# Optimization experiments

Hardware: AMD Instinct MI355X
Metric: run time of the kernel (lower is better)

## Reference

```python
import jax, jax.numpy as jnp
import numpy as np

B, SQ, SK, H, NH = 2, 2048, 2048, 1024, 16
HD = H // NH  # 64


def setup_inputs() -> dict:
    key = jax.random.key(0)
    ks = jax.random.split(key, 12)
    s = 1.0 / np.sqrt(H)
    inp = {
        "query": jax.random.normal(ks[0], (B, SQ, H), jnp.float32),
        "key": jax.random.normal(ks[1], (B, SK, H), jnp.float32),
        "value": jax.random.normal(ks[2], (B, SK, H), jnp.float32),
        # lower-triangular causal mask [B, SQ, SK]; nonzero = attend
        "causal_mask": jnp.broadcast_to(
            jnp.tril(jnp.ones((SQ, SK), jnp.int32)), (B, SQ, SK)
        ),
        "Wq": jax.random.uniform(ks[3], (H, H), jnp.float32, -s, s),
        "bq": jnp.zeros((H,), jnp.float32),
        "Wk": jax.random.uniform(ks[4], (H, H), jnp.float32, -s, s),
        "bk": jnp.zeros((H,), jnp.float32),
        "Wv": jax.random.uniform(ks[5], (H, H), jnp.float32, -s, s),
        "bv": jnp.zeros((H,), jnp.float32),
        "Wo": jax.random.uniform(ks[6], (H, H), jnp.float32, -s, s),
        "bo": jnp.zeros((H,), jnp.float32),
        "ln_g": jnp.ones((H,), jnp.float32),
        "ln_b": jnp.zeros((H,), jnp.float32),
    }
    return inp


def _layer_norm(x, g, b, eps=1e-5):
    mu = jnp.mean(x, axis=-1, keepdims=True)
    var = jnp.var(x, axis=-1, keepdims=True)
    return (x - mu) * jax.lax.rsqrt(var + eps) * g + b


def reference(query, key, value, causal_mask, Wq, bq, Wk, bk, Wv, bv, Wo, bo, ln_g, ln_b):
    # projections (torch Linear: x @ W.T + b)
    q = (query @ Wq.T + bq).reshape(B, SQ, NH, HD)
    k = (key @ Wk.T + bk).reshape(B, SK, NH, HD)
    v = (value @ Wv.T + bv).reshape(B, SK, NH, HD)
    # scores [B, NH, SQ, SK]
    scores = jnp.einsum("bqhd,bkhd->bhqk", q, k) / np.sqrt(HD).astype(np.float32)
    scores = jnp.where(causal_mask[:, None, :, :] == 0, -jnp.inf, scores)
    attn = jax.nn.softmax(scores, axis=-1)
    # dropout is identity in eval mode
    out = jnp.einsum("bhqk,bkhd->bqhd", attn, v).reshape(B, SQ, H)
    out = out @ Wo.T + bo
    return _layer_norm(query + out, ln_g, ln_b)
```

## Files before the change

kernel.cpp:

```cpp
#include <hip/hip_runtime.h>
#include <hip/hip_bf16.h>

#define SQL 2048
#define SKL 2048
#define HH  1024
#define NHH 16
#define HDD 64
#define BB  2
#define MM  (BB*SQL)

typedef __attribute__((ext_vector_type(8))) short short8;
typedef __attribute__((ext_vector_type(4))) short short4v;
typedef __attribute__((ext_vector_type(4))) float f32x4;
typedef unsigned short u16;

__device__ inline u16 f2bf(float f) {
    unsigned int u = __float_as_uint(f);
    u += 0x7fffu + ((u >> 16) & 1u);
    return (u16)(u >> 16);
}

__device__ inline void gl_lds16(const void* g, void* l) {
    __builtin_amdgcn_global_load_lds(
        (const __attribute__((address_space(1))) unsigned int*)g,
        (__attribute__((address_space(3))) unsigned int*)l, 16, 0, 0);
}

__global__ __launch_bounds__(256) void cvt_all_kernel(
    const float* __restrict__ q, const float* __restrict__ k, const float* __restrict__ v,
    const float* __restrict__ wq, const float* __restrict__ wk,
    const float* __restrict__ wv, const float* __restrict__ wo,
    u16* __restrict__ xq, u16* __restrict__ xk, u16* __restrict__ xv,
    u16* __restrict__ wqb, u16* __restrict__ wkb, u16* __restrict__ wvb, u16* __restrict__ wob)
{
    int b = blockIdx.x;
    const float* src; u16* dst;
    if      (b < 4096)  { src = q;  dst = xq; }
    else if (b < 8192)  { src = k;  dst = xk;  b -= 4096; }
    else if (b < 12288) { src = v;  dst = xv;  b -= 8192; }
    else if (b < 13312) { src = wq; dst = wqb; b -= 12288; }
    else if (b < 14336) { src = wk; dst = wkb; b -= 13312; }
    else if (b < 15360) { src = wv; dst = wvb; b -= 14336; }
    else                { src = wo; dst = wob; b -= 15360; }
    int i = (b * 256 + threadIdx.x) * 4;
    float4 vv = *(const float4*)(src + i);
    ushort4 oo;
    oo.x = f2bf(vv.x); oo.y = f2bf(vv.y); oo.z = f2bf(vv.z); oo.w = f2bf(vv.w);
    *(ushort4*)(dst + i) = oo;
}

__global__ __launch_bounds__(256) void proj_kernel(
    const u16* __restrict__ xq, const u16* __restrict__ xk, const u16* __restrict__ xv,
    const u16* __restrict__ wqb, const u16* __restrict__ wkb, const u16* __restrict__ wvb,
    const float* __restrict__ bq, const float* __restrict__ bk, const float* __restrict__ bv,
    u16* __restrict__ oq, u16* __restrict__ ok, u16* __restrict__ ov)
{
    const int z = blockIdx.z;
    const u16* A      = (z == 0) ? xq  : (z == 1) ? xk  : xv;
    const u16* W      = (z == 0) ? wqb : (z == 1) ? wkb : wvb;
    const float* bias = (z == 0) ? bq  : (z == 1) ? bk  : bv;
    u16* outb         = (z == 0) ? oq  : (z == 1) ? ok  : ov;
    const float scale = (z == 0) ? 0.125f * 1.4426950408889634f : 1.0f;

    __shared__ u16 lds_a[128 * 64];
    __shared__ u16 lds_b[128 * 64];

    const int t = threadIdx.x;
    const int lane = t & 63;
    const int quad = lane >> 4;
    const int lo = lane & 15;
    const int wv = t >> 6;
    const int wm = (wv >> 1) * 64, wn = (wv & 1) * 64;
    const int m0 = blockIdx.x * 128;
    const int n0 = blockIdx.y * 128;

    f32x4 acc[4][4];
#pragma unroll
    for (int i = 0; i < 4; i++)
#pragma unroll
        for (int j = 0; j < 4; j++) acc[i][j] = (f32x4){0.f, 0.f, 0.f, 0.f};

    int rr[4], cc[4];
#pragma unroll
    for (int u = 0; u < 4; u++) {
        int sl = u * 256 + t;
        rr[u] = sl >> 3;
        cc[u] = ((sl & 7) ^ (rr[u] & 7)) * 8;
    }

    for (int k0 = 0; k0 < HH; k0 += 64) {
#pragma unroll
        for (int u = 0; u < 4; u++) {
            gl_lds16(A + (size_t)(m0 + rr[u]) * HH + k0 + cc[u], &lds_a[(u * 256 + t) * 8]);
            gl_lds16(W + (size_t)(n0 + rr[u]) * HH + k0 + cc[u], &lds_b[(u * 256 + t) * 8]);
        }
        __syncthreads();
#pragma unroll
        for (int kk = 0; kk < 2; kk++) {
            short8 af[4], bf[4];
#pragma unroll
            for (int i = 0; i < 4; i++) {
                const int ra = wm + i * 16 + lo;
                const int rb = wn + i * 16 + lo;
                af[i] = *(const short8*)&lds_a[ra * 64 + (((kk * 4 + quad) ^ (ra & 7)) * 8)];
                bf[i] = *(const short8*)&lds_b[rb * 64 + (((kk * 4 + quad) ^ (rb & 7)) * 8)];
            }
            if (z == 2) {
#pragma unroll
                for (int i = 0; i < 4; i++)
#pragma unroll
                    for (int j = 0; j < 4; j++)
                        acc[i][j] = __builtin_amdgcn_mfma_f32_16x16x32_bf16(bf[j], af[i], acc[i][j], 0, 0, 0);
            } else {
#pragma unroll
                for (int i = 0; i < 4; i++)
#pragma unroll
                    for (int j = 0; j < 4; j++)
                        acc[i][j] = __builtin_amdgcn_mfma_f32_16x16x32_bf16(af[i], bf[j], acc[i][j], 0, 0, 0);
            }
        }
        __syncthreads();
    }

#pragma unroll
    for (int i = 0; i < 4; i++) {
#pragma unroll
        for (int j = 0; j < 4; j++) {
#pragma unroll
            for (int r = 0; r < 4; r++) {
                if (z == 2) {
                    int dg  = n0 + wn + j * 16 + quad * 4 + r;
                    int tok = m0 + wm + i * 16 + lo;
                    float val = acc[i][j][r] + bias[dg];
                    int head = dg >> 6, d = dg & 63;
                    int bi = tok >> 11, s = tok & 2047;
                    outb[(((size_t)bi * NHH + head) * HDD + d) * SKL + s] = f2bf(val);
                } else {
                    int row = m0 + wm + i * 16 + quad * 4 + r;
                    int col = n0 + wn + j * 16 + lo;
                    float val = (acc[i][j][r] + bias[col]) * scale;
                    int bi = row >> 11, s = row & 2047;
                    int head = col >> 6, d = col & 63;
                    outb[(((size_t)bi * NHH + head) * SQL + s) * HDD + d] = f2bf(val);
                }
            }
        }
    }
}

__global__ __launch_bounds__(256) void outproj_kernel(
    const u16* __restrict__ A, const u16* __restrict__ W,
    const float* __restrict__ bias, const float* __restrict__ resid,
    float* __restrict__ outf)
{
    __shared__ u16 lds_a[128 * 64];
    __shared__ u16 lds_b[128 * 64];

    const int t = threadIdx.x;
    const int lane = t & 63;
    const int quad = lane >> 4;
    const int lo = lane & 15;
    const int wv = t >> 6;
    const int wm = (wv >> 1) * 64, wn = (wv & 1) * 64;
    const int m0 = blockIdx.x * 128;
    const int n0 = blockIdx.y * 128;

    f32x4 acc[4][4];
#pragma unroll
    for (int i = 0; i < 4; i++)
#pragma unroll
        for (int j = 0; j < 4; j++) acc[i][j] = (f32x4){0.f, 0.f, 0.f, 0.f};

    int rr[4], cc[4];
#pragma unroll
    for (int u = 0; u < 4; u++) {
        int sl = u * 256 + t;
        rr[u] = sl >> 3;
        cc[u] = ((sl & 7) ^ (rr[u] & 7)) * 8;
    }

    for (int k0 = 0; k0 < HH; k0 += 64) {
#pragma unroll
        for (int u = 0; u < 4; u++) {
            gl_lds16(A + (size_t)(m0 + rr[u]) * HH + k0 + cc[u], &lds_a[(u * 256 + t) * 8]);
            gl_lds16(W + (size_t)(n0 + rr[u]) * HH + k0 + cc[u], &lds_b[(u * 256 + t) * 8]);
        }
        __syncthreads();
#pragma unroll
        for (int kk = 0; kk < 2; kk++) {
            short8 af[4], bf[4];
#pragma unroll
            for (int i = 0; i < 4; i++) {
                const int ra = wm + i * 16 + lo;
                const int rb = wn + i * 16 + lo;
                af[i] = *(const short8*)&lds_a[ra * 64 + (((kk * 4 + quad) ^ (ra & 7)) * 8)];
                bf[i] = *(const short8*)&lds_b[rb * 64 + (((kk * 4 + quad) ^ (rb & 7)) * 8)];
            }
#pragma unroll
            for (int i = 0; i < 4; i++)
#pragma unroll
                for (int j = 0; j < 4; j++)
                    acc[i][j] = __builtin_amdgcn_mfma_f32_16x16x32_bf16(af[i], bf[j], acc[i][j], 0, 0, 0);
        }
        __syncthreads();
    }

#pragma unroll
    for (int i = 0; i < 4; i++)
#pragma unroll
        for (int j = 0; j < 4; j++)
#pragma unroll
            for (int r = 0; r < 4; r++) {
                int row = m0 + wm + i * 16 + quad * 4 + r;
                int col = n0 + wn + j * 16 + lo;
                float val = acc[i][j][r] + bias[col] + resid[(size_t)row * HH + col];
                outf[(size_t)row * HH + col] = val;
            }
}

#define PSTR 72

__global__ __launch_bounds__(256) void attn_kernel(
    const u16* __restrict__ qb, const u16* __restrict__ kb, const u16* __restrict__ vtb,
    u16* __restrict__ attn_out)
{
    __shared__ u16 k_lds[64 * 64];
    __shared__ u16 vt_lds[64 * 64];
    __shared__ u16 p_lds[4 * 16 * PSTR];

    const int t = threadIdx.x;
    const int lane = t & 63;
    const int quad = lane >> 4;
    const int lo = lane & 15;
    const int w = t >> 6;
    const int qt = (SQL / 64 - 1) - (blockIdx.x >> 5);
    const int bh = blockIdx.x & 31;
    const int q0 = qt * 64;

    const u16* qbase = qb + ((size_t)bh * SQL + q0 + w * 16 + lo) * HDD + quad * 8;
    short8 qf0 = *(const short8*)qbase;
    short8 qf1 = *(const short8*)(qbase + 32);

    float m_s = -__builtin_inff(), l_s = 0.f;
    f32x4 o[4];
#pragma unroll
    for (int j = 0; j < 4; j++) o[j] = (f32x4){0.f, 0.f, 0.f, 0.f};

    const int sl0 = t, sl1 = 256 + t;
    const int r0 = sl0 >> 3, c0 = ((sl0 & 7) ^ (r0 & 7)) * 8;
    const int r1 = sl1 >> 3, c1 = ((sl1 & 7) ^ (r1 & 7)) * 8;
    const u16* kbh = kb + (size_t)bh * SKL * HDD;
    const u16* vbh = vtb + (size_t)bh * HDD * SKL;
    u16* ppriv = &p_lds[w * 16 * PSTR];

    for (int kt = 0; kt <= qt; kt++) {
        const int k0 = kt * 64;
        gl_lds16(kbh + (size_t)(k0 + r0) * HDD + c0, &k_lds[sl0 * 8]);
        gl_lds16(kbh + (size_t)(k0 + r1) * HDD + c1, &k_lds[sl1 * 8]);
        gl_lds16(vbh + (size_t)r0 * SKL + k0 + c0, &vt_lds[sl0 * 8]);
        gl_lds16(vbh + (size_t)r1 * SKL + k0 + c1, &vt_lds[sl1 * 8]);
        __syncthreads();

        f32x4 s[4];
        __builtin_amdgcn_s_setprio(1);
#pragma unroll
        for (int nt = 0; nt < 4; nt++) {
            const int row = nt * 16 + lo;
            short8 kf0 = *(const short8*)&k_lds[row * 64 + ((quad ^ (row & 7)) * 8)];
            short8 kf1 = *(const short8*)&k_lds[row * 64 + (((4 + quad) ^ (row & 7)) * 8)];
            s[nt] = (f32x4){0.f, 0.f, 0.f, 0.f};
            s[nt] = __builtin_amdgcn_mfma_f32_16x16x32_bf16(kf0, qf0, s[nt], 0, 0, 0);
            s[nt] = __builtin_amdgcn_mfma_f32_16x16x32_bf16(kf1, qf1, s[nt], 0, 0, 0);
        }
        __builtin_amdgcn_s_setprio(0);
        if (kt == qt) {
            const int ql = w * 16 + lo;
#pragma unroll
            for (int nt = 0; nt < 4; nt++)
#pragma unroll
                for (int r = 0; r < 4; r++)
                    if (nt * 16 + quad * 4 + r > ql) s[nt][r] = -__builtin_inff();
        }

        float mx = s[0][0];
#pragma unroll
        for (int nt = 0; nt < 4; nt++)
#pragma unroll
            for (int r = 0; r < 4; r++) mx = fmaxf(mx, s[nt][r]);
        mx = fmaxf(mx, __shfl_xor(mx, 16));
        mx = fmaxf(mx, __shfl_xor(mx, 32));

        if (!__all(mx - m_s <= 8.0f)) {
            float mnew = fmaxf(m_s, mx);
            float al = __builtin_amdgcn_exp2f(m_s - mnew);
            m_s = mnew;
            l_s *= al;
            float alr[4];
#pragma unroll
            for (int r = 0; r < 4; r++) alr[r] = __shfl(al, quad * 4 + r, 16);
#pragma unroll
            for (int nt = 0; nt < 4; nt++)
#pragma unroll
                for (int r = 0; r < 4; r++) o[nt][r] *= alr[r];
        }

        float rs = 0.f;
#pragma unroll
        for (int nt = 0; nt < 4; nt++)
#pragma unroll
            for (int r = 0; r < 4; r++) {
                s[nt][r] = __builtin_amdgcn_exp2f(s[nt][r] - m_s);
                rs += s[nt][r];
            }
        rs += __shfl_xor(rs, 16);
        rs += __shfl_xor(rs, 32);
        l_s += rs;

#pragma unroll
        for (int nt = 0; nt < 4; nt++) {
            short4v pk;
#pragma unroll
            for (int r = 0; r < 4; r++) pk[r] = (short)f2bf(s[nt][r]);
            *(short4v*)&ppriv[lo * PSTR + nt * 16 + quad * 4] = pk;
        }
        short8 pf0 = *(const short8*)&ppriv[lo * PSTR + quad * 8];
        short8 pf1 = *(const short8*)&ppriv[lo * PSTR + 32 + quad * 8];

        __builtin_amdgcn_s_setprio(1);
#pragma unroll
        for (int nt = 0; nt < 4; nt++) {
            const int row = nt * 16 + lo;
            short8 vf0 = *(const short8*)&vt_lds[row * 64 + ((quad ^ (row & 7)) * 8)];
            short8 vf1 = *(const short8*)&vt_lds[row * 64 + (((4 + quad) ^ (row & 7)) * 8)];
            o[nt] = __builtin_amdgcn_mfma_f32_16x16x32_bf16(pf0, vf0, o[nt], 0, 0, 0);
            o[nt] = __builtin_amdgcn_mfma_f32_16x16x32_bf16(pf1, vf1, o[nt], 0, 0, 0);
        }
        __builtin_amdgcn_s_setprio(0);
        __syncthreads();
    }

    const int b = bh >> 4, h = bh & 15;
    float inv[4];
#pragma unroll
    for (int r = 0; r < 4; r++) inv[r] = 1.0f / __shfl(l_s, quad * 4 + r, 16);
#pragma unroll
    for (int nt = 0; nt < 4; nt++)
#pragma unroll
        for (int r = 0; r < 4; r++) {
            int srow = q0 + w * 16 + quad * 4 + r;
            attn_out[((size_t)b * SQL + srow) * HH + h * HDD + nt * 16 + lo] =
                f2bf(o[nt][r] * inv[r]);
        }
}

__global__ __launch_bounds__(256) void ln_kernel(const float* __restrict__ x,
                                                 const float* __restrict__ g,
                                                 const float* __restrict__ bb,
                                                 float* __restrict__ out)
{
    const int row = blockIdx.x;
    const int t = threadIdx.x;
    const float* xr = x + (size_t)row * HH;
    float4 v = *(const float4*)(xr + t * 4);
    float s1 = v.x + v.y + v.z + v.w;
    float s2 = v.x * v.x + v.y * v.y + v.z * v.z + v.w * v.w;
#pragma unroll
    for (int off = 32; off; off >>= 1) { s1 += __shfl_xor(s1, off); s2 += __shfl_xor(s2, off); }
    __shared__ float red[8];
    if ((t & 63) == 0) { red[(t >> 6) * 2] = s1; red[(t >> 6) * 2 + 1] = s2; }
    __syncthreads();
    s1 = red[0] + red[2] + red[4] + red[6];
    s2 = red[1] + red[3] + red[5] + red[7];
    float mu = s1 * (1.0f / HH);
    float var = s2 * (1.0f / HH) - mu * mu;
    float rstd = rsqrtf(var + 1e-5f);
    float4 gg = *(const float4*)(g + t * 4);
    float4 b4 = *(const float4*)(bb + t * 4);
    float4 o;
    o.x = (v.x - mu) * rstd * gg.x + b4.x;
    o.y = (v.y - mu) * rstd * gg.y + b4.y;
    o.z = (v.z - mu) * rstd * gg.z + b4.z;
    o.w = (v.w - mu) * rstd * gg.w + b4.w;
    *(float4*)(out + (size_t)row * HH + t * 4) = o;
}

extern "C" void kernel_launch(void* const* d_in, const int* in_sizes, int n_in,
                              void* d_out, int out_size, void* d_ws, size_t ws_size,
                              hipStream_t stream)
{
    const float* query = (const float*)d_in[0];
    const float* key   = (const float*)d_in[1];
    const float* value = (const float*)d_in[2];
    const float* Wq = (const float*)d_in[4];
    const float* bq = (const float*)d_in[5];
    const float* Wk = (const float*)d_in[6];
    const float* bk = (const float*)d_in[7];
    const float* Wv = (const float*)d_in[8];
    const float* bv = (const float*)d_in[9];
    const float* Wo = (const float*)d_in[10];
    const float* bo = (const float*)d_in[11];
    const float* ln_g = (const float*)d_in[12];
    const float* ln_b = (const float*)d_in[13];
    float* out = (float*)d_out;

    char* wp = (char*)d_ws;
    auto alloc = [&](size_t bytes) { void* p = (void*)wp; wp += (bytes + 255) & ~(size_t)255; return p; };
    const int nW = HH * HH;
    const int nX = MM * HH;
    u16* wqb = (u16*)alloc((size_t)nW * 2);
    u16* wkb = (u16*)alloc((size_t)nW * 2);
    u16* wvb = (u16*)alloc((size_t)nW * 2);
    u16* wob = (u16*)alloc((size_t)nW * 2);
    u16* xq  = (u16*)alloc((size_t)nX * 2);
    u16* xk  = (u16*)alloc((size_t)nX * 2);
    u16* xv  = (u16*)alloc((size_t)nX * 2);
    u16* qbuf = (u16*)alloc((size_t)nX * 2);
    u16* kbuf = (u16*)alloc((size_t)nX * 2);
    u16* vbuf = (u16*)alloc((size_t)nX * 2);
    u16* attnb = (u16*)alloc((size_t)nX * 2);
    float* projf = (float*)alloc((size_t)nX * 4);

    cvt_all_kernel<<<16384, 256, 0, stream>>>(query, key, value, Wq, Wk, Wv, Wo,
                                              xq, xk, xv, wqb, wkb, wvb, wob);

    proj_kernel<<<dim3(32, 8, 3), 256, 0, stream>>>(
        xq, xk, xv, wqb, wkb, wvb, bq, bk, bv, qbuf, kbuf, vbuf);

    attn_kernel<<<1024, 256, 0, stream>>>(qbuf, kbuf, vbuf, attnb);

    outproj_kernel<<<dim3(32, 8), 256, 0, stream>>>(attnb, wob, bo, query, projf);

    ln_kernel<<<MM, 256, 0, stream>>>(projf, ln_g, ln_b, out);
}
```

Before: 269.8 us.

## Stage GEMM epilogues through LDS for vectorized stores; simplify attention rescale

The projection and output-projection epilogues now write accumulators into per-wave LDS tiles (XOR-swizzled), then read them back to issue 16-byte vectorized global stores and residual loads, where before each element was stored separately and the V-transpose store was strided. The MFMA operand order is swapped so the accumulator layout suits each epilogue. In attention, the lazy (thresholded) rescale of the running max is replaced by an unconditional rescale every tile, and the s_setprio hints are removed. This trades extra LDS traffic and barriers in the epilogue for coalesced memory writes, and adds per-tile multiply work in attention.

```diff
diff --git a/kernel.cpp b/kernel.cpp
--- a/kernel.cpp
+++ b/kernel.cpp
@@ -18,6 +18,13 @@
     unsigned int u = __float_as_uint(f);
     u += 0x7fffu + ((u >> 16) & 1u);
     return (u16)(u >> 16);
+}
+
+__device__ inline unsigned int bf2_bits(float a, float b) {
+    __hip_bfloat162 h = __float22bfloat162_rn(make_float2(a, b));
+    unsigned int r;
+    __builtin_memcpy(&r, &h, 4);
+    return r;
 }
 
 __device__ inline void gl_lds16(const void* g, void* l) {
@@ -62,8 +69,9 @@
     u16* outb         = (z == 0) ? oq  : (z == 1) ? ok  : ov;
     const float scale = (z == 0) ? 0.125f * 1.4426950408889634f : 1.0f;
 
-    __shared__ u16 lds_a[128 * 64];
-    __shared__ u16 lds_b[128 * 64];
+    __shared__ u16 pool[2 * 128 * 64];
+    u16* lds_a = pool;
+    u16* lds_b = pool + 128 * 64;
 
     const int t = threadIdx.x;
     const int lane = t & 63;
@@ -110,40 +118,73 @@
                 for (int i = 0; i < 4; i++)
 #pragma unroll
                     for (int j = 0; j < 4; j++)
+                        acc[i][j] = __builtin_amdgcn_mfma_f32_16x16x32_bf16(af[i], bf[j], acc[i][j], 0, 0, 0);
+            } else {
+#pragma unroll
+                for (int i = 0; i < 4; i++)
+#pragma unroll
+                    for (int j = 0; j < 4; j++)
                         acc[i][j] = __builtin_amdgcn_mfma_f32_16x16x32_bf16(bf[j], af[i], acc[i][j], 0, 0, 0);
-            } else {
-#pragma unroll
-                for (int i = 0; i < 4; i++)
-#pragma unroll
-                    for (int j = 0; j < 4; j++)
-                        acc[i][j] = __builtin_amdgcn_mfma_f32_16x16x32_bf16(af[i], bf[j], acc[i][j], 0, 0, 0);
-            }
-        }
-        __syncthreads();
-    }
-
-#pragma unroll
-    for (int i = 0; i < 4; i++) {
+            }
+        }
+        __syncthreads();
+    }
+
+    u16* cbuf = &pool[wv * 4096];
+
+    if (z != 2) {
 #pragma unroll
         for (int j = 0; j < 4; j++) {
-#pragma unroll
-            for (int r = 0; r < 4; r++) {
-                if (z == 2) {
-                    int dg  = n0 + wn + j * 16 + quad * 4 + r;
-                    int tok = m0 + wm + i * 16 + lo;
-                    float val = acc[i][j][r] + bias[dg];
-                    int head = dg >> 6, d = dg & 63;
-                    int bi = tok >> 11, s = tok & 2047;
-                    outb[(((size_t)bi * NHH + head) * HDD + d) * SKL + s] = f2bf(val);
-                } else {
-                    int row = m0 + wm + i * 16 + quad * 4 + r;
-                    int col = n0 + wn + j * 16 + lo;
-                    float val = (acc[i][j][r] + bias[col]) * scale;
-                    int bi = row >> 11, s = row & 2047;
-                    int head = col >> 6, d = col & 63;
-                    outb[(((size_t)bi * NHH + head) * SQL + s) * HDD + d] = f2bf(val);
-                }
-            }
+            float4 b4 = *(const float4*)&bias[n0 + wn + j * 16 + quad * 4];
+#pragma unroll
+            for (int i = 0; i < 4; i++) {
+                int tokl = i * 16 + lo;
+                int lc = j * 2 + (quad >> 1);
+                int phys = lc ^ (tokl & 7);
+                uint2 pk;
+                pk.x = bf2_bits((acc[i][j][0] + b4.x) * scale, (acc[i][j][1] + b4.y) * scale);
+                pk.y = bf2_bits((acc[i][j][2] + b4.z) * scale, (acc[i][j][3] + b4.w) * scale);
+                *(uint2*)&cbuf[tokl * 64 + phys * 8 + (quad & 1) * 4] = pk;
+            }
+        }
+        __syncthreads();
+#pragma unroll
+        for (int it = 0; it < 8; it++) {
+            int row = it * 8 + (lane >> 3);
+            int lc2 = lane & 7;
+            short8 val = *(const short8*)&cbuf[row * 64 + ((lc2 ^ (row & 7)) * 8)];
+            int tok = m0 + wm + row;
+            int dgb = n0 + wn + lc2 * 8;
+            int bi = tok >> 11, s = tok & 2047;
+            int head = dgb >> 6, d = dgb & 63;
+            *(short8*)&outb[(((size_t)bi * NHH + head) * SQL + s) * HDD + d] = val;
+        }
+    } else {
+#pragma unroll
+        for (int j = 0; j < 4; j++) {
+            float bsc = bias[n0 + wn + j * 16 + lo];
+#pragma unroll
+            for (int i = 0; i < 4; i++) {
+                int dgl = j * 16 + lo;
+                int lc = i * 2 + (quad >> 1);
+                int phys = lc ^ (dgl & 7);
+                uint2 pk;
+                pk.x = bf2_bits(acc[i][j][0] + bsc, acc[i][j][1] + bsc);
+                pk.y = bf2_bits(acc[i][j][2] + bsc, acc[i][j][3] + bsc);
+                *(uint2*)&cbuf[dgl * 64 + phys * 8 + (quad & 1) * 4] = pk;
+            }
+        }
+        __syncthreads();
+#pragma unroll
+        for (int it = 0; it < 8; it++) {
+            int row = it * 8 + (lane >> 3);
+            int lc2 = lane & 7;
+            short8 val = *(const short8*)&cbuf[row * 64 + ((lc2 ^ (row & 7)) * 8)];
+            int dg = n0 + wn + row;
+            int tokb = m0 + wm + lc2 * 8;
+            int bi = tokb >> 11, s = tokb & 2047;
+            int head = dg >> 6, d = dg & 63;
+            *(short8*)&outb[(((size_t)bi * NHH + head) * HDD + d) * SKL + s] = val;
         }
     }
 }
@@ -153,8 +194,9 @@
     const float* __restrict__ bias, const float* __restrict__ resid,
     float* __restrict__ outf)
 {
-    __shared__ u16 lds_a[128 * 64];
-    __shared__ u16 lds_b[128 * 64];
+    __shared__ u16 pool[2 * 128 * 64];
+    u16* lds_a = pool;
+    u16* lds_b = pool + 128 * 64;
 
     const int t = threadIdx.x;
     const int lane = t & 63;
@@ -200,22 +242,46 @@
             for (int i = 0; i < 4; i++)
 #pragma unroll
                 for (int j = 0; j < 4; j++)
-                    acc[i][j] = __builtin_amdgcn_mfma_f32_16x16x32_bf16(af[i], bf[j], acc[i][j], 0, 0, 0);
-        }
-        __syncthreads();
-    }
-
-#pragma unroll
-    for (int i = 0; i < 4; i++)
-#pragma unroll
-        for (int j = 0; j < 4; j++)
-#pragma unroll
-            for (int r = 0; r < 4; r++) {
-                int row = m0 + wm + i * 16 + quad * 4 + r;
-                int col = n0 + wn + j * 16 + lo;
-                float val = acc[i][j][r] + bias[col] + resid[(size_t)row * HH + col];
-                outf[(size_t)row * HH + col] = val;
-            }
+                    acc[i][j] = __builtin_amdgcn_mfma_f32_16x16x32_bf16(bf[j], af[i], acc[i][j], 0, 0, 0);
+        }
+        __syncthreads();
+    }
+
+    float* cbuf = (float*)&pool[wv * 4096];
+
+#pragma unroll
+    for (int half = 0; half < 2; half++) {
+#pragma unroll
+        for (int j = 0; j < 4; j++) {
+            float4 b4 = *(const float4*)&bias[n0 + wn + j * 16 + quad * 4];
+#pragma unroll
+            for (int ii = 0; ii < 2; ii++) {
+                int i = half * 2 + ii;
+                int tl = ii * 16 + lo;
+                int lc = j * 4 + quad;
+                int phys = lc ^ (tl & 7);
+                f32x4 vq;
+                vq[0] = acc[i][j][0] + b4.x; vq[1] = acc[i][j][1] + b4.y;
+                vq[2] = acc[i][j][2] + b4.z; vq[3] = acc[i][j][3] + b4.w;
+                *(f32x4*)&cbuf[tl * 64 + phys * 4] = vq;
+            }
+        }
+        __syncthreads();
+#pragma unroll
+        for (int it = 0; it < 8; it++) {
+            int rowl = it * 4 + (lane >> 4);
+            int lc2 = lane & 15;
+            f32x4 val = *(const f32x4*)&cbuf[rowl * 64 + ((lc2 ^ (rowl & 7)) * 4)];
+            int tok = m0 + wm + half * 32 + rowl;
+            int col = n0 + wn + lc2 * 4;
+            const float4 rd = *(const float4*)&resid[(size_t)tok * HH + col];
+            float4 o;
+            o.x = val[0] + rd.x; o.y = val[1] + rd.y;
+            o.z = val[2] + rd.z; o.w = val[3] + rd.w;
+            *(float4*)&outf[(size_t)tok * HH + col] = o;
+        }
+        __syncthreads();
+    }
 }
 
 #define PSTR 72
@@ -262,7 +328,6 @@
         __syncthreads();
 
         f32x4 s[4];
-        __builtin_amdgcn_s_setprio(1);
 #pragma unroll
         for (int nt = 0; nt < 4; nt++) {
             const int row = nt * 16 + lo;
@@ -272,7 +337,6 @@
             s[nt] = __builtin_amdgcn_mfma_f32_16x16x32_bf16(kf0, qf0, s[nt], 0, 0, 0);
             s[nt] = __builtin_amdgcn_mfma_f32_16x16x32_bf16(kf1, qf1, s[nt], 0, 0, 0);
         }
-        __builtin_amdgcn_s_setprio(0);
         if (kt == qt) {
             const int ql = w * 16 + lo;
 #pragma unroll
@@ -289,21 +353,9 @@
             for (int r = 0; r < 4; r++) mx = fmaxf(mx, s[nt][r]);
         mx = fmaxf(mx, __shfl_xor(mx, 16));
         mx = fmaxf(mx, __shfl_xor(mx, 32));
-
-        if (!__all(mx - m_s <= 8.0f)) {
-            float mnew = fmaxf(m_s, mx);
-            float al = __builtin_amdgcn_exp2f(m_s - mnew);
-            m_s = mnew;
-            l_s *= al;
-            float alr[4];
-#pragma unroll
-            for (int r = 0; r < 4; r++) alr[r] = __shfl(al, quad * 4 + r, 16);
-#pragma unroll
-            for (int nt = 0; nt < 4; nt++)
-#pragma unroll
-                for (int r = 0; r < 4; r++) o[nt][r] *= alr[r];
-        }
-
+        float mnew = fmaxf(m_s, mx);
+        float al = __builtin_amdgcn_exp2f(m_s - mnew);
+        m_s = mnew;
         float rs = 0.f;
 #pragma unroll
         for (int nt = 0; nt < 4; nt++)
@@ -314,7 +366,15 @@
             }
         rs += __shfl_xor(rs, 16);
         rs += __shfl_xor(rs, 32);
-        l_s += rs;
+        l_s = l_s * al + rs;
+
+        float alr[4];
+#pragma unroll
+        for (int r = 0; r < 4; r++) alr[r] = __shfl(al, quad * 4 + r, 16);
+#pragma unroll
+        for (int nt = 0; nt < 4; nt++)
+#pragma unroll
+            for (int r = 0; r < 4; r++) o[nt][r] *= alr[r];
 
 #pragma unroll
         for (int nt = 0; nt < 4; nt++) {
@@ -326,7 +386,6 @@
         short8 pf0 = *(const short8*)&ppriv[lo * PSTR + quad * 8];
         short8 pf1 = *(const short8*)&ppriv[lo * PSTR + 32 + quad * 8];
 
-        __builtin_amdgcn_s_setprio(1);
 #pragma unroll
         for (int nt = 0; nt < 4; nt++) {
             const int row = nt * 16 + lo;
@@ -335,7 +394,6 @@
             o[nt] = __builtin_amdgcn_mfma_f32_16x16x32_bf16(pf0, vf0, o[nt], 0, 0, 0);
             o[nt] = __builtin_amdgcn_mfma_f32_16x16x32_bf16(pf1, vf1, o[nt], 0, 0, 0);
         }
-        __builtin_amdgcn_s_setprio(0);
         __syncthreads();
     }
 
```

Result: faster. 253.9 us (-5.9%).
